# Performance work log

Measured on AMD Instinct MI355X. Metric: run time of the kernel, lower is better.

Reference implementation:

```python
import jax, jax.numpy as jnp
import numpy as np

N_NODES, N_EDGES = 100000, 1600000
D_IN, D_HID, D_OUT = 128, 128, 64


def setup_inputs() -> dict:
    key = jax.random.key(0)
    k = jax.random.split(key, 6)
    x = jax.random.normal(k[0], (N_NODES, D_IN), dtype=jnp.float32)
    edge_index = jax.random.randint(k[1], (2, N_EDGES), 0, N_NODES, dtype=jnp.int32)
    # GCNConv params: W stored as [in, out] for right-multiply, glorot-ish scale
    W1 = jax.random.normal(k[2], (D_IN, D_HID), dtype=jnp.float32) * (1.0 / np.sqrt(D_IN))
    b1 = jnp.zeros((D_HID,), dtype=jnp.float32)
    W2 = jax.random.normal(k[3], (D_HID, D_OUT), dtype=jnp.float32) * (1.0 / np.sqrt(D_HID))
    b2 = jnp.zeros((D_OUT,), dtype=jnp.float32)
    return {"x": x, "edge_index": edge_index, "W1": W1, "b1": b1, "W2": W2, "b2": b2}


def reference(x, edge_index, W1, b1, W2, b2):
    N = x.shape[0]
    loops = jnp.arange(N, dtype=edge_index.dtype)
    src = jnp.concatenate([edge_index[0], loops])  # [E+N]
    dst = jnp.concatenate([edge_index[1], loops])  # [E+N]
    # symmetric GCN normalization (deg over targets, incl. self loops)
    deg = jax.ops.segment_sum(jnp.ones_like(dst, dtype=x.dtype), dst, num_segments=N)
    dinv = jnp.where(deg > 0, jax.lax.rsqrt(deg), 0.0)
    norm = dinv[src] * dinv[dst]  # [E+N]

    def gcn(h, W, b):
        h = h @ W                         # [N, out]
        msg = h[src] * norm[:, None]      # gather + scale, [E+N, out]
        return jax.ops.segment_sum(msg, dst, num_segments=N) + b

    h = jax.nn.relu(gcn(x, W1, b1))  # Dropout is identity in eval
    return gcn(h, W2, b2)
```

## Files before the change

### kernel.cpp

```cpp
#include <hip/hip_runtime.h>


#define D_IN  128
#define D_HID 128
#define D_OUT 64
#define NBSHIFT 9

typedef short short8 __attribute__((ext_vector_type(8)));
typedef float floatx4 __attribute__((ext_vector_type(4)));

__device__ __forceinline__ unsigned short f2bf(float f) {
    unsigned int u = __float_as_uint(f);
    u += 0x7fffu + ((u >> 16) & 1u);
    return (unsigned short)(u >> 16);
}
__device__ __forceinline__ float bf2f(unsigned short h) {
    return __uint_as_float((unsigned int)h << 16);
}
__device__ __forceinline__ float bf_lo(unsigned int u) { return __uint_as_float(u << 16); }
__device__ __forceinline__ float bf_hi(unsigned int u) { return __uint_as_float(u & 0xffff0000u); }


__global__ __launch_bounds__(256) void k_zero_int(int* __restrict__ p, int n) {
    int i = blockIdx.x * 256 + threadIdx.x;
    if (i < n) p[i] = 0;
}

__global__ __launch_bounds__(256) void k_bhist(const int* __restrict__ dst,
                                               int* __restrict__ bcnt, int E, int NB) {
    __shared__ int h[256];
    const int t = threadIdx.x;
    h[t] = 0;
    __syncthreads();
    const int base = blockIdx.x * 8192;
#pragma unroll
    for (int k = 0; k < 32; ++k) {
        int e = base + k * 256 + t;
        if (e < E) atomicAdd(&h[dst[e] >> NBSHIFT], 1);
    }
    __syncthreads();
    if (t < NB && h[t]) atomicAdd(&bcnt[t], h[t]);
}

__global__ __launch_bounds__(256) void k_bscan(const int* __restrict__ bcnt,
                                               int* __restrict__ bbase,
                                               int* __restrict__ bcur, int NB, int E) {
    __shared__ int ls[256];
    const int t = threadIdx.x;
    int v = (t < NB) ? bcnt[t] : 0;
    ls[t] = v;
    __syncthreads();
    for (int off = 1; off < 256; off <<= 1) {
        int y = (t >= off) ? ls[t - off] : 0;
        __syncthreads();
        ls[t] += y;
        __syncthreads();
    }
    if (t < NB) {
        bbase[t] = ls[t] - v;
        bcur[t]  = ls[t] - v;
    }
    if (t == 0) bbase[NB] = E;
}

__global__ __launch_bounds__(256) void k_bin(const int* __restrict__ src,
                                             const int* __restrict__ dst,
                                             int2* __restrict__ ebuf,
                                             int* __restrict__ bcur, int E, int NB) {
    __shared__ int h[256];
    __shared__ int basep[256];
    const int t = threadIdx.x;
    h[t] = 0;
    __syncthreads();
    const int base = blockIdx.x * 4096;
    int s[16], d[16];
#pragma unroll
    for (int k = 0; k < 16; ++k) {
        int e = base + k * 256 + t;
        bool v = e < E;
        s[k] = v ? src[e] : 0;
        d[k] = v ? dst[e] : -1;
        if (v) atomicAdd(&h[d[k] >> NBSHIFT], 1);
    }
    __syncthreads();
    if (t < NB && h[t]) basep[t] = atomicAdd(&bcur[t], h[t]);
    __syncthreads();
    h[t] = 0;
    __syncthreads();
#pragma unroll
    for (int k = 0; k < 16; ++k) {
        if (d[k] >= 0) {
            int b = d[k] >> NBSHIFT;
            int r = atomicAdd(&h[b], 1);
            ebuf[basep[b] + r] = make_int2(s[k], d[k]);
        }
    }
}

__global__ __launch_bounds__(256) void k_bfill(const int2* __restrict__ ebuf,
                                               const int* __restrict__ bbase,
                                               int* __restrict__ csr,
                                               int* __restrict__ rowstart,
                                               float* __restrict__ dinv,
                                               int N, int NB, int E) {
    __shared__ int cnt[512];
    __shared__ int pref[512];
    __shared__ int tsum[256];
    const int t = threadIdx.x;
    const int b = blockIdx.x;
    const int nb0 = b << NBSHIFT;
    const int NN = min(512, N - nb0);
    const int e0 = bbase[b], e1 = bbase[b + 1];

    cnt[t] = 0;
    cnt[t + 256] = 0;
    __syncthreads();
    for (int e = e0 + t; e < e1; e += 256)
        atomicAdd(&cnt[ebuf[e].y - nb0], 1);
    __syncthreads();

    int a0 = cnt[2 * t], a1 = cnt[2 * t + 1];
    tsum[t] = a0 + a1;
    __syncthreads();
    for (int off = 1; off < 256; off <<= 1) {
        int y = (t >= off) ? tsum[t - off] : 0;
        __syncthreads();
        tsum[t] += y;
        __syncthreads();
    }
    int excl = tsum[t] - (a0 + a1);
    pref[2 * t] = excl;
    pref[2 * t + 1] = excl + a0;
    __syncthreads();

    for (int nl = t; nl < NN; nl += 256) {
        rowstart[nb0 + nl] = e0 + pref[nl];
        dinv[nb0 + nl] = rsqrtf((float)(cnt[nl] + 1));
    }
    if (b == NB - 1 && t == 0) rowstart[N] = E;
    __syncthreads();

    for (int e = e0 + t; e < e1; e += 256) {
        int2 ed = ebuf[e];
        int r = atomicAdd(&pref[ed.y - nb0], 1);
        csr[e0 + r] = ed.x;
    }
}

__global__ void k_zero_pad(unsigned short* __restrict__ h1b,
                           unsigned short* __restrict__ h2b, int N) {
    int t = threadIdx.x;
    if (t < 128) h1b[(size_t)N * 128 + t] = 0;
    if (t < 64)  h2b[(size_t)N * 64 + t] = 0;
}


template <int DOUT_>
__global__ __launch_bounds__(256) void k_wsplit(const float* __restrict__ W,
                                                unsigned short* __restrict__ Ws) {
    constexpr int NCT = DOUT_ / 16;
    constexpr int HALF = 4 * NCT * 64 * 8;
    int id = blockIdx.x * 256 + threadIdx.x;
    if (id >= HALF) return;
    int i = id & 7;
    int lane = (id >> 3) & 63;
    int ctkt = id >> 9;
    int ct = ctkt % NCT, kt = ctkt / NCT;
    int k = kt * 32 + ((lane >> 4) << 3) + i;
    int n = ct * 16 + (lane & 15);
    float v = W[(size_t)k * DOUT_ + n];
    unsigned short h = f2bf(v);
    Ws[id] = h;
    Ws[HALF + id] = f2bf(v - bf2f(h));
}


template <int DOUT_>
__global__ __launch_bounds__(256) void mfma_gemm(const float* __restrict__ X,
                                                 const unsigned short* __restrict__ Wsplit,
                                                 const float* __restrict__ dinv,
                                                 unsigned short* __restrict__ Hb,
                                                 int N) {
    constexpr int NCT = DOUT_ / 16;
    constexpr int HALF = 4 * NCT * 64 * 8;
    __shared__ unsigned short lds[2 * HALF];

    const int t = threadIdx.x;
    {
        const int4* s4 = (const int4*)Wsplit;
        int4* d4 = (int4*)lds;
        constexpr int NV = 2 * HALF / 8;
        for (int i = t; i < NV; i += 256) d4[i] = s4[i];
    }
    __syncthreads();

    const int wave = t >> 6, lane = t & 63;
    const int grow = blockIdx.x * 64 + wave * 16 + (lane & 15);
    const int rowc = min(grow, N - 1);
    const int kl = (lane >> 4) << 3;

    floatx4 acc[NCT];
#pragma unroll
    for (int c = 0; c < NCT; ++c) acc[c] = (floatx4)0.f;

#pragma unroll
    for (int kt = 0; kt < 4; ++kt) {
        const float* xp = X + (size_t)rowc * 128 + kt * 32 + kl;
        float4 a0 = *(const float4*)xp;
        float4 a1 = *(const float4*)(xp + 4);
        float xs[8] = {a0.x, a0.y, a0.z, a0.w, a1.x, a1.y, a1.z, a1.w};
        short8 ah, al;
#pragma unroll
        for (int i = 0; i < 8; ++i) {
            unsigned short h = f2bf(xs[i]);
            ah[i] = (short)h;
            al[i] = (short)f2bf(xs[i] - bf2f(h));
        }
#pragma unroll
        for (int c = 0; c < NCT; ++c) {
            const int off = ((kt * NCT + c) * 64 + lane) * 8;
            short8 bh = *(const short8*)&lds[off];
            short8 bl = *(const short8*)&lds[HALF + off];
            acc[c] = __builtin_amdgcn_mfma_f32_16x16x32_bf16(ah, bh, acc[c], 0, 0, 0);
            acc[c] = __builtin_amdgcn_mfma_f32_16x16x32_bf16(al, bh, acc[c], 0, 0, 0);
            acc[c] = __builtin_amdgcn_mfma_f32_16x16x32_bf16(ah, bl, acc[c], 0, 0, 0);
        }
    }

    const int orow = blockIdx.x * 64 + wave * 16 + ((lane >> 4) << 2);
#pragma unroll
    for (int r = 0; r < 4; ++r) {
        int gr = orow + r;
        if (gr < N) {
            float dn = dinv[gr];
#pragma unroll
            for (int c = 0; c < NCT; ++c)
                Hb[(size_t)gr * DOUT_ + c * 16 + (lane & 15)] = f2bf(acc[c][r] * dn);
        }
    }
}


__global__ __launch_bounds__(256) void agg1_kernel(const unsigned int* __restrict__ Hb,
                                                   const int* __restrict__ rowstart,
                                                   const int* __restrict__ csr_src,
                                                   const float* __restrict__ dinv,
                                                   const float* __restrict__ bias,
                                                   float* __restrict__ out, int N) {
    const int wid = (blockIdx.x * 256 + threadIdx.x) >> 6;
    const int lane = threadIdx.x & 63;
    if (wid >= N) return;
    const int e0 = rowstart[wid], e1 = rowstart[wid + 1];

    float accx = 0.f, accy = 0.f;
    for (int eb = e0; eb < e1; eb += 64) {
        int myE = eb + lane;
        int s_l = (myE < e1) ? csr_src[myE] : N;
        int nbatch = min(64, e1 - eb);
        for (int i = 0; i < nbatch; i += 8) {
            int s[8]; unsigned int u[8];
#pragma unroll
            for (int j = 0; j < 8; ++j) s[j] = __shfl(s_l, i + j);
#pragma unroll
            for (int j = 0; j < 8; ++j) u[j] = Hb[(size_t)s[j] * 64 + lane];
#pragma unroll
            for (int j = 0; j < 8; ++j) {
                accx += bf_lo(u[j]);
                accy += bf_hi(u[j]);
            }
        }
    }
    unsigned int us = Hb[(size_t)wid * 64 + lane];
    accx += bf_lo(us);
    accy += bf_hi(us);
    const float dn = dinv[wid];
    accx = fmaf(accx, dn, bias[lane * 2 + 0]);
    accy = fmaf(accy, dn, bias[lane * 2 + 1]);
    accx = fmaxf(accx, 0.f);
    accy = fmaxf(accy, 0.f);
    reinterpret_cast<float2*>(out)[(size_t)wid * 64 + lane] = make_float2(accx, accy);
}

__global__ __launch_bounds__(256) void agg2_kernel(const unsigned short* __restrict__ Hb,
                                                   const int* __restrict__ rowstart,
                                                   const int* __restrict__ csr_src,
                                                   const float* __restrict__ dinv,
                                                   const float* __restrict__ bias,
                                                   float* __restrict__ out, int N) {
    const int wid = (blockIdx.x * 256 + threadIdx.x) >> 6;
    const int lane = threadIdx.x & 63;
    if (wid >= N) return;
    const int e0 = rowstart[wid], e1 = rowstart[wid + 1];

    float acc = 0.f;
    for (int eb = e0; eb < e1; eb += 64) {
        int myE = eb + lane;
        int s_l = (myE < e1) ? csr_src[myE] : N;
        int nbatch = min(64, e1 - eb);
        for (int i = 0; i < nbatch; i += 8) {
            int s[8]; unsigned short h[8];
#pragma unroll
            for (int j = 0; j < 8; ++j) s[j] = __shfl(s_l, i + j);
#pragma unroll
            for (int j = 0; j < 8; ++j) h[j] = Hb[(size_t)s[j] * 64 + lane];
#pragma unroll
            for (int j = 0; j < 8; ++j)
                acc += __uint_as_float((unsigned int)h[j] << 16);
        }
    }
    acc += __uint_as_float((unsigned int)Hb[(size_t)wid * 64 + lane] << 16);
    acc = fmaf(acc, dinv[wid], bias[lane]);
    out[(size_t)wid * 64 + lane] = acc;
}


extern "C" void kernel_launch(void* const* d_in, const int* in_sizes, int n_in,
                              void* d_out, int out_size, void* d_ws, size_t ws_size,
                              hipStream_t stream) {
    const float* x  = (const float*)d_in[0];
    const int*   ei = (const int*)d_in[1];
    const float* W1 = (const float*)d_in[2];
    const float* b1 = (const float*)d_in[3];
    const float* W2 = (const float*)d_in[4];
    const float* b2 = (const float*)d_in[5];
    float* out = (float*)d_out;

    const int N = in_sizes[0] / D_IN;
    const int E = in_sizes[1] / 2;
    const int* src = ei;
    const int* dst = ei + E;
    const int NB = (N + 511) >> NBSHIFT;

    char* w = (char*)d_ws;
    auto alloc = [&](size_t bytes) {
        char* p = w;
        w += (bytes + 255) & ~(size_t)255;
        return p;
    };
    int*   rowstart  = (int*)alloc((size_t)(N + 1) * 4);
    float* dinv      = (float*)alloc((size_t)N * 4);
    int*   csr       = (int*)alloc((size_t)E * 4);
    unsigned short* h1b = (unsigned short*)alloc((size_t)(N + 1) * D_HID * 2);
    unsigned short* h2b = (unsigned short*)alloc((size_t)(N + 1) * D_OUT * 2);
    float* hg        = (float*)alloc((size_t)N * D_HID * 4);
    int*   bcnt      = (int*)alloc((size_t)NB * 4);
    int*   bbase     = (int*)alloc((size_t)(NB + 1) * 4);
    int*   bcur      = (int*)alloc((size_t)NB * 4);
    unsigned short* w1s = (unsigned short*)alloc(2 * 4 * (D_HID / 16) * 64 * 8 * 2);
    unsigned short* w2s = (unsigned short*)alloc(2 * 4 * (D_OUT / 16) * 64 * 8 * 2);
    int2*  ebuf      = (int2*)hg;

    k_zero_int<<<1, 256, 0, stream>>>(bcnt, NB);
    k_bhist<<<(E + 8191) / 8192, 256, 0, stream>>>(dst, bcnt, E, NB);
    k_bscan<<<1, 256, 0, stream>>>(bcnt, bbase, bcur, NB, E);
    k_bin<<<(E + 4095) / 4096, 256, 0, stream>>>(src, dst, ebuf, bcur, E, NB);
    k_bfill<<<NB, 256, 0, stream>>>(ebuf, bbase, csr, rowstart, dinv, N, NB, E);
    k_zero_pad<<<1, 128, 0, stream>>>(h1b, h2b, N);
    k_wsplit<D_HID><<<(4 * (D_HID / 16) * 64 * 8 + 255) / 256, 256, 0, stream>>>(W1, w1s);
    k_wsplit<D_OUT><<<(4 * (D_OUT / 16) * 64 * 8 + 255) / 256, 256, 0, stream>>>(W2, w2s);

    mfma_gemm<D_HID><<<(N + 63) / 64, 256, 0, stream>>>(x, w1s, dinv, h1b, N);
    agg1_kernel<<<(N + 3) / 4, 256, 0, stream>>>((const unsigned int*)h1b, rowstart, csr,
                                                 dinv, b1, hg, N);
    mfma_gemm<D_OUT><<<(N + 63) / 64, 256, 0, stream>>>(hg, w2s, dinv, h2b, N);
    agg2_kernel<<<(N + 3) / 4, 256, 0, stream>>>(h2b, rowstart, csr, dinv, b2, out, N);
}
```

Baseline: 221.5 us.

## Pack multiple nodes per wave in aggregation with 16-byte vector gathers

Both aggregation kernels now assign several destination nodes to each wave (4 nodes in layer 1, 8 in layer 2). Each node gets a 16- or 8-lane subgroup that gathers neighbour rows with 16-byte uint4 loads instead of 4- or 2-byte per-lane loads. This cuts the number of memory instructions per edge and raises the bytes moved per load, aiming at the gather-bound aggregation cost. The trade-off is divergence: every subgroup loops to the maximum degree among the nodes in its wave, so work is wasted on padding edges that read the zero pad row.

```diff
diff --git a/kernel.cpp b/kernel.cpp
--- a/kernel.cpp
+++ b/kernel.cpp
@@ -241,76 +241,123 @@
 }
 
 
-__global__ __launch_bounds__(256) void agg1_kernel(const unsigned int* __restrict__ Hb,
+__global__ __launch_bounds__(256) void agg1_kernel(const uint4* __restrict__ H4,
                                                    const int* __restrict__ rowstart,
                                                    const int* __restrict__ csr_src,
                                                    const float* __restrict__ dinv,
                                                    const float* __restrict__ bias,
                                                    float* __restrict__ out, int N) {
-    const int wid = (blockIdx.x * 256 + threadIdx.x) >> 6;
-    const int lane = threadIdx.x & 63;
-    if (wid >= N) return;
-    const int e0 = rowstart[wid], e1 = rowstart[wid + 1];
-
-    float accx = 0.f, accy = 0.f;
-    for (int eb = e0; eb < e1; eb += 64) {
-        int myE = eb + lane;
-        int s_l = (myE < e1) ? csr_src[myE] : N;
-        int nbatch = min(64, e1 - eb);
-        for (int i = 0; i < nbatch; i += 8) {
-            int s[8]; unsigned int u[8];
-#pragma unroll
-            for (int j = 0; j < 8; ++j) s[j] = __shfl(s_l, i + j);
-#pragma unroll
-            for (int j = 0; j < 8; ++j) u[j] = Hb[(size_t)s[j] * 64 + lane];
-#pragma unroll
-            for (int j = 0; j < 8; ++j) {
-                accx += bf_lo(u[j]);
-                accy += bf_hi(u[j]);
+    const int t = threadIdx.x;
+    const int wave = t >> 6, lane = t & 63;
+    const int g = lane >> 4, gl = lane & 15;
+    const int n = blockIdx.x * 16 + wave * 4 + g;
+    const bool live = n < N;
+    const int e0 = live ? rowstart[n] : 0;
+    const int e1 = live ? rowstart[n + 1] : 0;
+    const int deg = e1 - e0;
+    int m = deg;
+    m = max(m, __shfl_xor(m, 16));
+    m = max(m, __shfl_xor(m, 32));
+
+    float acc[8] = {0.f, 0.f, 0.f, 0.f, 0.f, 0.f, 0.f, 0.f};
+    for (int eb = 0; eb < m; eb += 16) {
+        int s_l = (eb + gl < deg) ? csr_src[e0 + eb + gl] : N;
+        for (int j = 0; j < 16 && eb + j < m; j += 4) {
+            int sj[4]; uint4 u[4];
+#pragma unroll
+            for (int q = 0; q < 4; ++q) sj[q] = __shfl(s_l, (g << 4) | (j + q));
+#pragma unroll
+            for (int q = 0; q < 4; ++q) u[q] = H4[(size_t)sj[q] * 16 + gl];
+#pragma unroll
+            for (int q = 0; q < 4; ++q) {
+                acc[0] += bf_lo(u[q].x); acc[1] += bf_hi(u[q].x);
+                acc[2] += bf_lo(u[q].y); acc[3] += bf_hi(u[q].y);
+                acc[4] += bf_lo(u[q].z); acc[5] += bf_hi(u[q].z);
+                acc[6] += bf_lo(u[q].w); acc[7] += bf_hi(u[q].w);
             }
         }
     }
-    unsigned int us = Hb[(size_t)wid * 64 + lane];
-    accx += bf_lo(us);
-    accy += bf_hi(us);
-    const float dn = dinv[wid];
-    accx = fmaf(accx, dn, bias[lane * 2 + 0]);
-    accy = fmaf(accy, dn, bias[lane * 2 + 1]);
-    accx = fmaxf(accx, 0.f);
-    accy = fmaxf(accy, 0.f);
-    reinterpret_cast<float2*>(out)[(size_t)wid * 64 + lane] = make_float2(accx, accy);
-}
-
-__global__ __launch_bounds__(256) void agg2_kernel(const unsigned short* __restrict__ Hb,
+    uint4 us = H4[(size_t)(live ? n : N) * 16 + gl];
+    acc[0] += bf_lo(us.x); acc[1] += bf_hi(us.x);
+    acc[2] += bf_lo(us.y); acc[3] += bf_hi(us.y);
+    acc[4] += bf_lo(us.z); acc[5] += bf_hi(us.z);
+    acc[6] += bf_lo(us.w); acc[7] += bf_hi(us.w);
+
+    if (live) {
+        const float dn = dinv[n];
+        float4 o0, o1;
+        o0.x = fmaxf(fmaf(acc[0], dn, bias[gl * 8 + 0]), 0.f);
+        o0.y = fmaxf(fmaf(acc[1], dn, bias[gl * 8 + 1]), 0.f);
+        o0.z = fmaxf(fmaf(acc[2], dn, bias[gl * 8 + 2]), 0.f);
+        o0.w = fmaxf(fmaf(acc[3], dn, bias[gl * 8 + 3]), 0.f);
+        o1.x = fmaxf(fmaf(acc[4], dn, bias[gl * 8 + 4]), 0.f);
+        o1.y = fmaxf(fmaf(acc[5], dn, bias[gl * 8 + 5]), 0.f);
+        o1.z = fmaxf(fmaf(acc[6], dn, bias[gl * 8 + 6]), 0.f);
+        o1.w = fmaxf(fmaf(acc[7], dn, bias[gl * 8 + 7]), 0.f);
+        float* op = out + (size_t)n * 128 + gl * 8;
+        *reinterpret_cast<float4*>(op) = o0;
+        *reinterpret_cast<float4*>(op + 4) = o1;
+    }
+}
+
+__global__ __launch_bounds__(256) void agg2_kernel(const uint4* __restrict__ H4,
                                                    const int* __restrict__ rowstart,
                                                    const int* __restrict__ csr_src,
                                                    const float* __restrict__ dinv,
                                                    const float* __restrict__ bias,
                                                    float* __restrict__ out, int N) {
-    const int wid = (blockIdx.x * 256 + threadIdx.x) >> 6;
-    const int lane = threadIdx.x & 63;
-    if (wid >= N) return;
-    const int e0 = rowstart[wid], e1 = rowstart[wid + 1];
-
-    float acc = 0.f;
-    for (int eb = e0; eb < e1; eb += 64) {
-        int myE = eb + lane;
-        int s_l = (myE < e1) ? csr_src[myE] : N;
-        int nbatch = min(64, e1 - eb);
-        for (int i = 0; i < nbatch; i += 8) {
-            int s[8]; unsigned short h[8];
-#pragma unroll
-            for (int j = 0; j < 8; ++j) s[j] = __shfl(s_l, i + j);
-#pragma unroll
-            for (int j = 0; j < 8; ++j) h[j] = Hb[(size_t)s[j] * 64 + lane];
-#pragma unroll
-            for (int j = 0; j < 8; ++j)
-                acc += __uint_as_float((unsigned int)h[j] << 16);
-        }
-    }
-    acc += __uint_as_float((unsigned int)Hb[(size_t)wid * 64 + lane] << 16);
-    acc = fmaf(acc, dinv[wid], bias[lane]);
-    out[(size_t)wid * 64 + lane] = acc;
+    const int t = threadIdx.x;
+    const int wave = t >> 6, lane = t & 63;
+    const int g = lane >> 3, gl = lane & 7;
+    const int n = blockIdx.x * 32 + wave * 8 + g;
+    const bool live = n < N;
+    const int e0 = live ? rowstart[n] : 0;
+    const int e1 = live ? rowstart[n + 1] : 0;
+    const int deg = e1 - e0;
+    int m = deg;
+    m = max(m, __shfl_xor(m, 8));
+    m = max(m, __shfl_xor(m, 16));
+    m = max(m, __shfl_xor(m, 32));
+
+    float acc[8] = {0.f, 0.f, 0.f, 0.f, 0.f, 0.f, 0.f, 0.f};
+    for (int eb = 0; eb < m; eb += 8) {
+        int s_l = (eb + gl < deg) ? csr_src[e0 + eb + gl] : N;
+        for (int j = 0; j < 8 && eb + j < m; j += 4) {
+            int sj[4]; uint4 u[4];
+#pragma unroll
+            for (int q = 0; q < 4; ++q) sj[q] = __shfl(s_l, (g << 3) | (j + q));
+#pragma unroll
+            for (int q = 0; q < 4; ++q) u[q] = H4[(size_t)sj[q] * 8 + gl];
+#pragma unroll
+            for (int q = 0; q < 4; ++q) {
+                acc[0] += bf_lo(u[q].x); acc[1] += bf_hi(u[q].x);
+                acc[2] += bf_lo(u[q].y); acc[3] += bf_hi(u[q].y);
+                acc[4] += bf_lo(u[q].z); acc[5] += bf_hi(u[q].z);
+                acc[6] += bf_lo(u[q].w); acc[7] += bf_hi(u[q].w);
+            }
+        }
+    }
+    uint4 us = H4[(size_t)(live ? n : N) * 8 + gl];
+    acc[0] += bf_lo(us.x); acc[1] += bf_hi(us.x);
+    acc[2] += bf_lo(us.y); acc[3] += bf_hi(us.y);
+    acc[4] += bf_lo(us.z); acc[5] += bf_hi(us.z);
+    acc[6] += bf_lo(us.w); acc[7] += bf_hi(us.w);
+
+    if (live) {
+        const float dn = dinv[n];
+        float4 o0, o1;
+        o0.x = fmaf(acc[0], dn, bias[gl * 8 + 0]);
+        o0.y = fmaf(acc[1], dn, bias[gl * 8 + 1]);
+        o0.z = fmaf(acc[2], dn, bias[gl * 8 + 2]);
+        o0.w = fmaf(acc[3], dn, bias[gl * 8 + 3]);
+        o1.x = fmaf(acc[4], dn, bias[gl * 8 + 4]);
+        o1.y = fmaf(acc[5], dn, bias[gl * 8 + 5]);
+        o1.z = fmaf(acc[6], dn, bias[gl * 8 + 6]);
+        o1.w = fmaf(acc[7], dn, bias[gl * 8 + 7]);
+        float* op = out + (size_t)n * 64 + gl * 8;
+        *reinterpret_cast<float4*>(op) = o0;
+        *reinterpret_cast<float4*>(op + 4) = o1;
+    }
 }
 
 
@@ -360,8 +407,9 @@
     k_wsplit<D_OUT><<<(4 * (D_OUT / 16) * 64 * 8 + 255) / 256, 256, 0, stream>>>(W2, w2s);
 
     mfma_gemm<D_HID><<<(N + 63) / 64, 256, 0, stream>>>(x, w1s, dinv, h1b, N);
-    agg1_kernel<<<(N + 3) / 4, 256, 0, stream>>>((const unsigned int*)h1b, rowstart, csr,
-                                                 dinv, b1, hg, N);
+    agg1_kernel<<<(N + 15) / 16, 256, 0, stream>>>((const uint4*)h1b, rowstart, csr,
+                                                   dinv, b1, hg, N);
     mfma_gemm<D_OUT><<<(N + 63) / 64, 256, 0, stream>>>(hg, w2s, dinv, h2b, N);
-    agg2_kernel<<<(N + 3) / 4, 256, 0, stream>>>(h2b, rowstart, csr, dinv, b2, out, N);
-}
+    agg2_kernel<<<(N + 31) / 32, 256, 0, stream>>>((const uint4*)h2b, rowstart, csr,
+                                                   dinv, b2, out, N);
+}
```

Result: faster. 213.7 us (-3.5%).
